# Kernel tuning notes

Hardware: AMD Instinct MI355X
Metric: run time of the kernel (lower is better)

Reference implementation:

```python
import jax, jax.numpy as jnp
import numpy as np

LOG2 = float(np.log(2.0))

def ssp(x):
    # shifted softplus: softplus(x) - log(2)
    return jax.nn.softplus(x) - LOG2

def setup_inputs() -> dict:
    key = jax.random.key(0)
    ks = jax.random.split(key, 16)
    N, E, F = 50000, 800000, 128  # atoms, interactions, feature/filter dim
    s = 0.05
    return {
        "x": jax.random.normal(ks[0], (N, F), jnp.float32),
        "dijk": jax.random.uniform(ks[1], (E, F), jnp.float32),
        "idx_j": jax.random.randint(ks[2], (E,), 0, N),
        "seg_i": jnp.sort(jax.random.randint(ks[3], (E,), 0, N)),
        "seg_j": jnp.arange(E),
        "seg_i_sum": N,
        "W1": jax.random.normal(ks[4], (F, F), jnp.float32) * s,
        "b1": jnp.zeros((F,), jnp.float32),
        "W2": jax.random.normal(ks[5], (F, F), jnp.float32) * s,
        "b2": jnp.zeros((F,), jnp.float32),
        "W_in2fac": jax.random.normal(ks[6], (F, F), jnp.float32) * s,
        "W_fac2out": jax.random.normal(ks[7], (F, F), jnp.float32) * s,
        "b_fac2out": jnp.zeros((F,), jnp.float32),
        "W_dense": jax.random.normal(ks[8], (F, F), jnp.float32) * s,
        "b_dense": jnp.zeros((F,), jnp.float32),
    }

def reference(x, dijk, idx_j, seg_i, seg_j, seg_i_sum,
              W1, b1, W2, b2, W_in2fac, W_fac2out, b_fac2out, W_dense, b_dense):
    E = dijk.shape[0]
    # --- CFnetFilter: dense -> dense -> segment-sum over seg_j ---
    h = ssp(dijk @ W1 + b1)                        # [E, F]
    w_ijk = ssp(h @ W2 + b2)                       # [E, F]
    w_ij = jax.ops.segment_sum(w_ijk, seg_j, num_segments=E)  # [E, F]
    # --- CFConv: in2fac -> gather idx_j -> filter mult -> segment-sum seg_i -> fac2out ---
    f = x @ W_in2fac                               # [N, F]
    f = f[idx_j]                                   # gather, [E, F]
    wf = w_ij * f                                  # [E, F]
    conv = jax.ops.segment_sum(wf, seg_i, num_segments=seg_i_sum)  # [N, F]
    c = ssp(conv @ W_fac2out + b_fac2out)          # [N, F]
    # --- residual dense ---
    v = c @ W_dense + b_dense                      # [N, F]
    y = x + v
    return (y, v)
```

## Files before the change

### kernel.cpp

```cpp
#include <hip/hip_runtime.h>
#include <hip/hip_bf16.h>

#define F 128

typedef __attribute__((ext_vector_type(8))) short bf16x8;
typedef __attribute__((ext_vector_type(4))) float f32x4;


__device__ __forceinline__ short f2bf(float f) {
  union { float f; unsigned u; } v; v.f = f;
  unsigned r = (v.u + 0x7FFFu + ((v.u >> 16) & 1u)) >> 16;
  return (short)r;
}

__device__ __forceinline__ float sspf(float x) {
  float t = __expf(-fabsf(x));
  return fmaxf(x, 0.0f) + __logf(1.0f + t) - 0.69314718055994530942f;
}

__device__ __forceinline__ int h_idx(int row, int k) {
  int chunk = k >> 3;
  int sw = chunk ^ (row & 15);
  return row * 128 + sw * 8 + (k & 7);
}

__device__ __forceinline__ int wf_idx(int row, int c) {
  return row * 128 + (c ^ ((row & 4) << 2));
}

__device__ __forceinline__ bf16x8 load_bfrag(const short* sW, int nt, int kb, int lane) {
  return *(const bf16x8*)(sW + (((nt * 4 + kb) * 64 + lane) << 3));
}

__device__ __forceinline__ bf16x8 load_afrag_f32(const float* __restrict__ p, bool valid) {
  bf16x8 a = {0, 0, 0, 0, 0, 0, 0, 0};
  if (valid) {
    const float4* q = (const float4*)p;
    float4 x0 = q[0], x1 = q[1];
    a[0] = f2bf(x0.x); a[1] = f2bf(x0.y); a[2] = f2bf(x0.z); a[3] = f2bf(x0.w);
    a[4] = f2bf(x1.x); a[5] = f2bf(x1.y); a[6] = f2bf(x1.z); a[7] = f2bf(x1.w);
  }
  return a;
}

__global__ void prep_weights(const float* __restrict__ W1, const float* __restrict__ W2,
                             const float* __restrict__ Wi2f, const float* __restrict__ Wf2o,
                             const float* __restrict__ Wd, unsigned short* __restrict__ out) {
  int t = blockIdx.x * 256 + threadIdx.x;
  int m = t >> 14;
  int idx = t & 16383;
  int k = idx >> 7, n = idx & 127;
  const float* W = (m == 0) ? W1 : (m == 1) ? W2 : (m == 2) ? Wi2f : (m == 3) ? Wf2o : Wd;
  float v = W[idx];
  int nt = n >> 4, kb = k >> 5;
  int lane = (((k >> 3) & 3) << 4) | (n & 15);
  int j = k & 7;
  int dst = (((nt * 4 + kb) * 64 + lane) << 3) | j;
  out[(m << 14) + dst] = (unsigned short)f2bf(v);
}

__global__ __launch_bounds__(256, 2) void f_kernel(const float* __restrict__ x,
                                                   const unsigned short* __restrict__ wfrag,
                                                   float* __restrict__ f, int N) {
  __shared__ union { short s[16384]; float4 v4[2048]; } sm;
  const int tid = threadIdx.x;
  const int lane = tid & 63, wv = tid >> 6;
  const int quad = lane >> 4, ln = lane & 15;
  const int r0 = blockIdx.x * 128;

  {
    const float4* src = (const float4*)(wfrag + 2 * 16384);
#pragma unroll
    for (int i = 0; i < 8; ++i) sm.v4[tid + 256 * i] = src[tid + 256 * i];
  }

  bf16x8 a1[2][4];
#pragma unroll
  for (int mt = 0; mt < 2; ++mt) {
    int row = r0 + wv * 32 + mt * 16 + ln;
    bool valid = row < N;
    const float* rp = x + (size_t)row * F + quad * 8;
#pragma unroll
    for (int kb = 0; kb < 4; ++kb) a1[mt][kb] = load_afrag_f32(rp + kb * 32, valid);
  }
  __syncthreads();

#pragma unroll
  for (int nt = 0; nt < 8; ++nt) {
    f32x4 acc0 = {0, 0, 0, 0}, acc1 = {0, 0, 0, 0};
#pragma unroll
    for (int kb = 0; kb < 4; ++kb) {
      bf16x8 b = load_bfrag(sm.s, nt, kb, lane);
      acc0 = __builtin_amdgcn_mfma_f32_16x16x32_bf16(a1[0][kb], b, acc0, 0, 0, 0);
      acc1 = __builtin_amdgcn_mfma_f32_16x16x32_bf16(a1[1][kb], b, acc1, 0, 0, 0);
    }
    int col = nt * 16 + ln;
#pragma unroll
    for (int mt = 0; mt < 2; ++mt) {
#pragma unroll
      for (int r = 0; r < 4; ++r) {
        int row = r0 + wv * 32 + mt * 16 + quad * 4 + r;
        if (row < N) f[(size_t)row * F + col] = (mt == 0) ? acc0[r] : acc1[r];
      }
    }
  }
}

__global__ __launch_bounds__(256, 2) void edge_kernel(
    const float* __restrict__ dijk, const int* __restrict__ idx_j, const int* __restrict__ seg_i,
    const float* __restrict__ b1, const float* __restrict__ b2,
    const unsigned short* __restrict__ wfrag, const float* __restrict__ f,
    float* __restrict__ conv, int E) {
  __shared__ union { short s[32768]; float fl[16384]; float4 v4[4096]; } sm;
  __shared__ int sIdx[128];
  __shared__ int sSeg[128];

  const int tid = threadIdx.x;
  const int lane = tid & 63, wv = tid >> 6;
  const int quad = lane >> 4, ln = lane & 15;
  const int e0 = blockIdx.x * 128;

  {
    const float4* src = (const float4*)wfrag;
#pragma unroll
    for (int i = 0; i < 16; ++i) sm.v4[tid + 256 * i] = src[tid + 256 * i];
  }
  if (tid < 128) {
    int e = e0 + tid;
    sIdx[tid] = (e < E) ? idx_j[e] : 0;
    sSeg[tid] = (e < E) ? seg_i[e] : -1;
  }

  float bias1v[8], bias2v[8];
#pragma unroll
  for (int nt = 0; nt < 8; ++nt) {
    bias1v[nt] = b1[nt * 16 + ln];
    bias2v[nt] = b2[nt * 16 + ln];
  }

  bf16x8 a1[2][4];
#pragma unroll
  for (int mt = 0; mt < 2; ++mt) {
    int row = e0 + wv * 32 + mt * 16 + ln;
    bool valid = row < E;
    const float* rp = dijk + (size_t)row * F + quad * 8;
#pragma unroll
    for (int kb = 0; kb < 4; ++kb) a1[mt][kb] = load_afrag_f32(rp + kb * 32, valid);
  }
  __syncthreads();

  short hreg[2][8][4];
  const short* sW1 = sm.s;
  const short* sW2 = sm.s + 16384;
#pragma unroll
  for (int nt = 0; nt < 8; ++nt) {
    f32x4 acc0 = {0, 0, 0, 0}, acc1 = {0, 0, 0, 0};
#pragma unroll
    for (int kb = 0; kb < 4; ++kb) {
      bf16x8 b = load_bfrag(sW1, nt, kb, lane);
      acc0 = __builtin_amdgcn_mfma_f32_16x16x32_bf16(a1[0][kb], b, acc0, 0, 0, 0);
      acc1 = __builtin_amdgcn_mfma_f32_16x16x32_bf16(a1[1][kb], b, acc1, 0, 0, 0);
    }
#pragma unroll
    for (int r = 0; r < 4; ++r) {
      hreg[0][nt][r] = f2bf(sspf(acc0[r] + bias1v[nt]));
      hreg[1][nt][r] = f2bf(sspf(acc1[r] + bias1v[nt]));
    }
  }
  __syncthreads();

  short* sH = sm.s;
#pragma unroll
  for (int mt = 0; mt < 2; ++mt)
#pragma unroll
    for (int nt = 0; nt < 8; ++nt)
#pragma unroll
      for (int r = 0; r < 4; ++r) {
        int row = wv * 32 + mt * 16 + quad * 4 + r;
        sH[h_idx(row, nt * 16 + ln)] = hreg[mt][nt][r];
      }
  __syncthreads();

  bf16x8 a2[2][4];
#pragma unroll
  for (int mt = 0; mt < 2; ++mt) {
    int row = wv * 32 + mt * 16 + ln;
#pragma unroll
    for (int kb = 0; kb < 4; ++kb)
      a2[mt][kb] = *(const bf16x8*)(sH + h_idx(row, kb * 32 + quad * 8));
  }

  float wreg[2][8][4];
#pragma unroll
  for (int nt = 0; nt < 8; ++nt) {
    f32x4 acc0 = {0, 0, 0, 0}, acc1 = {0, 0, 0, 0};
#pragma unroll
    for (int kb = 0; kb < 4; ++kb) {
      bf16x8 b = load_bfrag(sW2, nt, kb, lane);
      acc0 = __builtin_amdgcn_mfma_f32_16x16x32_bf16(a2[0][kb], b, acc0, 0, 0, 0);
      acc1 = __builtin_amdgcn_mfma_f32_16x16x32_bf16(a2[1][kb], b, acc1, 0, 0, 0);
    }
#pragma unroll
    for (int r = 0; r < 4; ++r) {
      wreg[0][nt][r] = sspf(acc0[r] + bias2v[nt]);
      wreg[1][nt][r] = sspf(acc1[r] + bias2v[nt]);
    }
  }
  __syncthreads();

  float* sWF = sm.fl;
#pragma unroll
  for (int mt = 0; mt < 2; ++mt)
#pragma unroll
    for (int r = 0; r < 4; ++r) {
      int rloc = wv * 32 + mt * 16 + quad * 4 + r;
      int jrow = sIdx[rloc];
      const float* fp = f + (size_t)jrow * F;
#pragma unroll
      for (int nt = 0; nt < 8; ++nt) {
        int c = nt * 16 + ln;
        sWF[wf_idx(rloc, c)] = wreg[mt][nt][r] * fp[c];
      }
    }
  __syncthreads();

  {
    int c = tid & 127;
    int half = tid >> 7;
    int r0 = half * 64;
    float acc = 0.0f;
    int cur = sSeg[r0];
    for (int r = r0; r < r0 + 64; ++r) {
      int s = sSeg[r];
      if (s != cur) {
        if (cur >= 0) atomicAdd(conv + (size_t)cur * F + c, acc);
        acc = 0.0f; cur = s;
      }
      acc += sWF[wf_idx(r, c)];
    }
    if (cur >= 0) atomicAdd(conv + (size_t)cur * F + c, acc);
  }
}

__global__ __launch_bounds__(256, 2) void node_kernel(
    const float* __restrict__ conv, const float* __restrict__ x,
    const float* __restrict__ bf2o, const float* __restrict__ bd,
    const unsigned short* __restrict__ wfrag, float* __restrict__ y,
    float* __restrict__ vout, int N) {
  __shared__ union { short s[32768]; float4 v4[4096]; } sm;
  const int tid = threadIdx.x;
  const int lane = tid & 63, wv = tid >> 6;
  const int quad = lane >> 4, ln = lane & 15;
  const int r0 = blockIdx.x * 128;

  {
    const float4* src = (const float4*)(wfrag + 3 * 16384);
#pragma unroll
    for (int i = 0; i < 16; ++i) sm.v4[tid + 256 * i] = src[tid + 256 * i];
  }

  float bfv[8], bdv[8];
#pragma unroll
  for (int nt = 0; nt < 8; ++nt) {
    bfv[nt] = bf2o[nt * 16 + ln];
    bdv[nt] = bd[nt * 16 + ln];
  }

  bf16x8 a1[2][4];
#pragma unroll
  for (int mt = 0; mt < 2; ++mt) {
    int row = r0 + wv * 32 + mt * 16 + ln;
    bool valid = row < N;
    const float* rp = conv + (size_t)row * F + quad * 8;
#pragma unroll
    for (int kb = 0; kb < 4; ++kb) a1[mt][kb] = load_afrag_f32(rp + kb * 32, valid);
  }
  __syncthreads();

  short creg[2][8][4];
  const short* sWa = sm.s;
  const short* sWd = sm.s + 16384;
#pragma unroll
  for (int nt = 0; nt < 8; ++nt) {
    f32x4 acc0 = {0, 0, 0, 0}, acc1 = {0, 0, 0, 0};
#pragma unroll
    for (int kb = 0; kb < 4; ++kb) {
      bf16x8 b = load_bfrag(sWa, nt, kb, lane);
      acc0 = __builtin_amdgcn_mfma_f32_16x16x32_bf16(a1[0][kb], b, acc0, 0, 0, 0);
      acc1 = __builtin_amdgcn_mfma_f32_16x16x32_bf16(a1[1][kb], b, acc1, 0, 0, 0);
    }
#pragma unroll
    for (int r = 0; r < 4; ++r) {
      creg[0][nt][r] = f2bf(sspf(acc0[r] + bfv[nt]));
      creg[1][nt][r] = f2bf(sspf(acc1[r] + bfv[nt]));
    }
  }
  __syncthreads();

  short* sC = sm.s;
#pragma unroll
  for (int mt = 0; mt < 2; ++mt)
#pragma unroll
    for (int nt = 0; nt < 8; ++nt)
#pragma unroll
      for (int r = 0; r < 4; ++r) {
        int row = wv * 32 + mt * 16 + quad * 4 + r;
        sC[h_idx(row, nt * 16 + ln)] = creg[mt][nt][r];
      }
  __syncthreads();

  bf16x8 a2[2][4];
#pragma unroll
  for (int mt = 0; mt < 2; ++mt) {
    int row = wv * 32 + mt * 16 + ln;
#pragma unroll
    for (int kb = 0; kb < 4; ++kb)
      a2[mt][kb] = *(const bf16x8*)(sC + h_idx(row, kb * 32 + quad * 8));
  }

#pragma unroll
  for (int nt = 0; nt < 8; ++nt) {
    f32x4 acc0 = {0, 0, 0, 0}, acc1 = {0, 0, 0, 0};
#pragma unroll
    for (int kb = 0; kb < 4; ++kb) {
      bf16x8 b = load_bfrag(sWd, nt, kb, lane);
      acc0 = __builtin_amdgcn_mfma_f32_16x16x32_bf16(a2[0][kb], b, acc0, 0, 0, 0);
      acc1 = __builtin_amdgcn_mfma_f32_16x16x32_bf16(a2[1][kb], b, acc1, 0, 0, 0);
    }
    int col = nt * 16 + ln;
#pragma unroll
    for (int mt = 0; mt < 2; ++mt) {
#pragma unroll
      for (int r = 0; r < 4; ++r) {
        int row = r0 + wv * 32 + mt * 16 + quad * 4 + r;
        if (row < N) {
          float v = ((mt == 0) ? acc0[r] : acc1[r]) + bdv[nt];
          size_t o = (size_t)row * F + col;
          y[o] = x[o] + v;
          vout[o] = v;
        }
      }
    }
  }
}

extern "C" void kernel_launch(void* const* d_in, const int* in_sizes, int n_in,
                              void* d_out, int out_size, void* d_ws, size_t ws_size,
                              hipStream_t stream) {
  const float* x    = (const float*)d_in[0];
  const float* dijk = (const float*)d_in[1];
  const int*   idxj = (const int*)d_in[2];
  const int*   segi = (const int*)d_in[3];
  const float* W1   = (const float*)d_in[6];
  const float* b1   = (const float*)d_in[7];
  const float* W2   = (const float*)d_in[8];
  const float* b2   = (const float*)d_in[9];
  const float* Wi2f = (const float*)d_in[10];
  const float* Wf2o = (const float*)d_in[11];
  const float* bf2o = (const float*)d_in[12];
  const float* Wd   = (const float*)d_in[13];
  const float* bd   = (const float*)d_in[14];

  int N = in_sizes[0] / F;
  int E = in_sizes[1] / F;

  unsigned short* wfrag = (unsigned short*)d_ws;
  float* fbuf = (float*)((char*)d_ws + 5 * 16384 * sizeof(unsigned short));
  float* conv = fbuf + (size_t)N * F;

  float* y = (float*)d_out;
  float* vout = y + (size_t)N * F;

  hipMemsetAsync(conv, 0, (size_t)N * F * sizeof(float), stream);
  prep_weights<<<320, 256, 0, stream>>>(W1, W2, Wi2f, Wf2o, Wd, wfrag);

  int nb = (N + 127) / 128;
  int eb = (E + 127) / 128;
  f_kernel<<<nb, 256, 0, stream>>>(x, wfrag, fbuf, N);
  edge_kernel<<<eb, 256, 0, stream>>>(dijk, idxj, segi, b1, b2, wfrag, fbuf, conv, E);
  node_kernel<<<nb, 256, 0, stream>>>(conv, x, bf2o, bd, wfrag, y, vout, N);
}
```

Baseline: 844.9 us.

## Read weight fragments from global memory and halve LDS to raise occupancy

```diff
diff --git a/kernel.cpp b/kernel.cpp
--- a/kernel.cpp
+++ b/kernel.cpp
@@ -1,5 +1,4 @@
 #include <hip/hip_runtime.h>
-#include <hip/hip_bf16.h>
 
 #define F 128
 
@@ -13,6 +12,12 @@
   return (short)r;
 }
 
+__device__ __forceinline__ unsigned cvt_pk_bf16(float a, float b) {
+  unsigned d;
+  asm("v_cvt_pk_bf16_f32 %0, %1, %2" : "=v"(d) : "v"(a), "v"(b));
+  return d;
+}
+
 __device__ __forceinline__ float sspf(float x) {
   float t = __expf(-fabsf(x));
   return fmaxf(x, 0.0f) + __logf(1.0f + t) - 0.69314718055994530942f;
@@ -24,23 +29,28 @@
   return row * 128 + sw * 8 + (k & 7);
 }
 
-__device__ __forceinline__ int wf_idx(int row, int c) {
+__device__ __forceinline__ int wfb_idx(int row, int c) {
   return row * 128 + (c ^ ((row & 4) << 2));
 }
 
-__device__ __forceinline__ bf16x8 load_bfrag(const short* sW, int nt, int kb, int lane) {
-  return *(const bf16x8*)(sW + (((nt * 4 + kb) * 64 + lane) << 3));
+__device__ __forceinline__ bf16x8 load_bfrag_g(const unsigned short* __restrict__ W,
+                                               int nt, int kb, int lane) {
+  return *(const bf16x8*)(W + (((nt * 4 + kb) * 64 + lane) << 3));
 }
 
 __device__ __forceinline__ bf16x8 load_afrag_f32(const float* __restrict__ p, bool valid) {
-  bf16x8 a = {0, 0, 0, 0, 0, 0, 0, 0};
+  union { bf16x8 v; unsigned u[4]; } r;
   if (valid) {
     const float4* q = (const float4*)p;
     float4 x0 = q[0], x1 = q[1];
-    a[0] = f2bf(x0.x); a[1] = f2bf(x0.y); a[2] = f2bf(x0.z); a[3] = f2bf(x0.w);
-    a[4] = f2bf(x1.x); a[5] = f2bf(x1.y); a[6] = f2bf(x1.z); a[7] = f2bf(x1.w);
-  }
-  return a;
+    r.u[0] = cvt_pk_bf16(x0.x, x0.y);
+    r.u[1] = cvt_pk_bf16(x0.z, x0.w);
+    r.u[2] = cvt_pk_bf16(x1.x, x1.y);
+    r.u[3] = cvt_pk_bf16(x1.z, x1.w);
+  } else {
+    r.u[0] = r.u[1] = r.u[2] = r.u[3] = 0u;
+  }
+  return r.v;
 }
 
 __global__ void prep_weights(const float* __restrict__ W1, const float* __restrict__ W2,
@@ -59,20 +69,14 @@
   out[(m << 14) + dst] = (unsigned short)f2bf(v);
 }
 
-__global__ __launch_bounds__(256, 2) void f_kernel(const float* __restrict__ x,
+__global__ __launch_bounds__(256, 4) void f_kernel(const float* __restrict__ x,
                                                    const unsigned short* __restrict__ wfrag,
                                                    float* __restrict__ f, int N) {
-  __shared__ union { short s[16384]; float4 v4[2048]; } sm;
   const int tid = threadIdx.x;
   const int lane = tid & 63, wv = tid >> 6;
   const int quad = lane >> 4, ln = lane & 15;
   const int r0 = blockIdx.x * 128;
-
-  {
-    const float4* src = (const float4*)(wfrag + 2 * 16384);
-#pragma unroll
-    for (int i = 0; i < 8; ++i) sm.v4[tid + 256 * i] = src[tid + 256 * i];
-  }
+  const unsigned short* Wf = wfrag + 2 * 16384;
 
   bf16x8 a1[2][4];
 #pragma unroll
@@ -83,14 +87,13 @@
 #pragma unroll
     for (int kb = 0; kb < 4; ++kb) a1[mt][kb] = load_afrag_f32(rp + kb * 32, valid);
   }
-  __syncthreads();
-
-#pragma unroll
-  for (int nt = 0; nt < 8; ++nt) {
-    f32x4 acc0 = {0, 0, 0, 0}, acc1 = {0, 0, 0, 0};
-#pragma unroll
-    for (int kb = 0; kb < 4; ++kb) {
-      bf16x8 b = load_bfrag(sm.s, nt, kb, lane);
+
+#pragma unroll
+  for (int nt = 0; nt < 8; ++nt) {
+    f32x4 acc0 = {0, 0, 0, 0}, acc1 = {0, 0, 0, 0};
+#pragma unroll
+    for (int kb = 0; kb < 4; ++kb) {
+      bf16x8 b = load_bfrag_g(Wf, nt, kb, lane);
       acc0 = __builtin_amdgcn_mfma_f32_16x16x32_bf16(a1[0][kb], b, acc0, 0, 0, 0);
       acc1 = __builtin_amdgcn_mfma_f32_16x16x32_bf16(a1[1][kb], b, acc1, 0, 0, 0);
     }
@@ -106,12 +109,12 @@
   }
 }
 
-__global__ __launch_bounds__(256, 2) void edge_kernel(
+__global__ __launch_bounds__(256, 4) void edge_kernel(
     const float* __restrict__ dijk, const int* __restrict__ idx_j, const int* __restrict__ seg_i,
     const float* __restrict__ b1, const float* __restrict__ b2,
     const unsigned short* __restrict__ wfrag, const float* __restrict__ f,
     float* __restrict__ conv, int E) {
-  __shared__ union { short s[32768]; float fl[16384]; float4 v4[4096]; } sm;
+  __shared__ union { short s[16384]; float fl[8192]; } sm;
   __shared__ int sIdx[128];
   __shared__ int sSeg[128];
 
@@ -119,12 +122,9 @@
   const int lane = tid & 63, wv = tid >> 6;
   const int quad = lane >> 4, ln = lane & 15;
   const int e0 = blockIdx.x * 128;
-
-  {
-    const float4* src = (const float4*)wfrag;
-#pragma unroll
-    for (int i = 0; i < 16; ++i) sm.v4[tid + 256 * i] = src[tid + 256 * i];
-  }
+  const unsigned short* W1f = wfrag;
+  const unsigned short* W2f = wfrag + 16384;
+
   if (tid < 128) {
     int e = e0 + tid;
     sIdx[tid] = (e < E) ? idx_j[e] : 0;
@@ -147,38 +147,26 @@
 #pragma unroll
     for (int kb = 0; kb < 4; ++kb) a1[mt][kb] = load_afrag_f32(rp + kb * 32, valid);
   }
-  __syncthreads();
-
-  short hreg[2][8][4];
-  const short* sW1 = sm.s;
-  const short* sW2 = sm.s + 16384;
-#pragma unroll
-  for (int nt = 0; nt < 8; ++nt) {
-    f32x4 acc0 = {0, 0, 0, 0}, acc1 = {0, 0, 0, 0};
-#pragma unroll
-    for (int kb = 0; kb < 4; ++kb) {
-      bf16x8 b = load_bfrag(sW1, nt, kb, lane);
+
+  short* sH = sm.s;
+#pragma unroll
+  for (int nt = 0; nt < 8; ++nt) {
+    f32x4 acc0 = {0, 0, 0, 0}, acc1 = {0, 0, 0, 0};
+#pragma unroll
+    for (int kb = 0; kb < 4; ++kb) {
+      bf16x8 b = load_bfrag_g(W1f, nt, kb, lane);
       acc0 = __builtin_amdgcn_mfma_f32_16x16x32_bf16(a1[0][kb], b, acc0, 0, 0, 0);
       acc1 = __builtin_amdgcn_mfma_f32_16x16x32_bf16(a1[1][kb], b, acc1, 0, 0, 0);
     }
+    int c = nt * 16 + ln;
 #pragma unroll
     for (int r = 0; r < 4; ++r) {
-      hreg[0][nt][r] = f2bf(sspf(acc0[r] + bias1v[nt]));
-      hreg[1][nt][r] = f2bf(sspf(acc1[r] + bias1v[nt]));
-    }
-  }
-  __syncthreads();
-
-  short* sH = sm.s;
-#pragma unroll
-  for (int mt = 0; mt < 2; ++mt)
-#pragma unroll
-    for (int nt = 0; nt < 8; ++nt)
-#pragma unroll
-      for (int r = 0; r < 4; ++r) {
-        int row = wv * 32 + mt * 16 + quad * 4 + r;
-        sH[h_idx(row, nt * 16 + ln)] = hreg[mt][nt][r];
-      }
+      sH[h_idx(wv * 32 + quad * 4 + r, c)] =
+          (short)cvt_pk_bf16(sspf(acc0[r] + bias1v[nt]), 0.0f);
+      sH[h_idx(wv * 32 + 16 + quad * 4 + r, c)] =
+          (short)cvt_pk_bf16(sspf(acc1[r] + bias1v[nt]), 0.0f);
+    }
+  }
   __syncthreads();
 
   bf16x8 a2[2][4];
@@ -196,7 +184,7 @@
     f32x4 acc0 = {0, 0, 0, 0}, acc1 = {0, 0, 0, 0};
 #pragma unroll
     for (int kb = 0; kb < 4; ++kb) {
-      bf16x8 b = load_bfrag(sW2, nt, kb, lane);
+      bf16x8 b = load_bfrag_g(W2f, nt, kb, lane);
       acc0 = __builtin_amdgcn_mfma_f32_16x16x32_bf16(a2[0][kb], b, acc0, 0, 0, 0);
       acc1 = __builtin_amdgcn_mfma_f32_16x16x32_bf16(a2[1][kb], b, acc1, 0, 0, 0);
     }
@@ -210,54 +198,55 @@
 
   float* sWF = sm.fl;
 #pragma unroll
-  for (int mt = 0; mt < 2; ++mt)
+  for (int half = 0; half < 2; ++half) {
 #pragma unroll
     for (int r = 0; r < 4; ++r) {
-      int rloc = wv * 32 + mt * 16 + quad * 4 + r;
-      int jrow = sIdx[rloc];
+      int lr = quad * 4 + r;
+      int brow = wv * 16 + lr;
+      int erow = wv * 32 + half * 16 + lr;
+      int jrow = sIdx[erow];
       const float* fp = f + (size_t)jrow * F;
 #pragma unroll
       for (int nt = 0; nt < 8; ++nt) {
         int c = nt * 16 + ln;
-        sWF[wf_idx(rloc, c)] = wreg[mt][nt][r] * fp[c];
+        sWF[wfb_idx(brow, c)] = wreg[half][nt][r] * fp[c];
       }
     }
-  __syncthreads();
-
-  {
-    int c = tid & 127;
-    int half = tid >> 7;
-    int r0 = half * 64;
-    float acc = 0.0f;
-    int cur = sSeg[r0];
-    for (int r = r0; r < r0 + 64; ++r) {
-      int s = sSeg[r];
-      if (s != cur) {
-        if (cur >= 0) atomicAdd(conv + (size_t)cur * F + c, acc);
-        acc = 0.0f; cur = s;
+    __syncthreads();
+
+    {
+      int c = tid & 127;
+      int sub = tid >> 7;
+      int b0 = sub * 32;
+      float acc = 0.0f;
+      int cur = sSeg[((b0 >> 4) << 5) + half * 16 + (b0 & 15)];
+      for (int b = b0; b < b0 + 32; ++b) {
+        int act = ((b >> 4) << 5) + half * 16 + (b & 15);
+        int s = sSeg[act];
+        if (s != cur) {
+          if (cur >= 0) atomicAdd(conv + (size_t)cur * F + c, acc);
+          acc = 0.0f; cur = s;
+        }
+        acc += sWF[wfb_idx(b, c)];
       }
-      acc += sWF[wf_idx(r, c)];
-    }
-    if (cur >= 0) atomicAdd(conv + (size_t)cur * F + c, acc);
-  }
-}
-
-__global__ __launch_bounds__(256, 2) void node_kernel(
+      if (cur >= 0) atomicAdd(conv + (size_t)cur * F + c, acc);
+    }
+    if (half == 0) __syncthreads();
+  }
+}
+
+__global__ __launch_bounds__(256, 4) void node_kernel(
     const float* __restrict__ conv, const float* __restrict__ x,
     const float* __restrict__ bf2o, const float* __restrict__ bd,
     const unsigned short* __restrict__ wfrag, float* __restrict__ y,
     float* __restrict__ vout, int N) {
-  __shared__ union { short s[32768]; float4 v4[4096]; } sm;
+  __shared__ short sC[16384];
   const int tid = threadIdx.x;
   const int lane = tid & 63, wv = tid >> 6;
   const int quad = lane >> 4, ln = lane & 15;
   const int r0 = blockIdx.x * 128;
-
-  {
-    const float4* src = (const float4*)(wfrag + 3 * 16384);
-#pragma unroll
-    for (int i = 0; i < 16; ++i) sm.v4[tid + 256 * i] = src[tid + 256 * i];
-  }
+  const unsigned short* Wa = wfrag + 3 * 16384;
+  const unsigned short* Wd = wfrag + 4 * 16384;
 
   float bfv[8], bdv[8];
 #pragma unroll
@@ -275,38 +264,25 @@
 #pragma unroll
     for (int kb = 0; kb < 4; ++kb) a1[mt][kb] = load_afrag_f32(rp + kb * 32, valid);
   }
-  __syncthreads();
-
-  short creg[2][8][4];
-  const short* sWa = sm.s;
-  const short* sWd = sm.s + 16384;
-#pragma unroll
-  for (int nt = 0; nt < 8; ++nt) {
-    f32x4 acc0 = {0, 0, 0, 0}, acc1 = {0, 0, 0, 0};
-#pragma unroll
-    for (int kb = 0; kb < 4; ++kb) {
-      bf16x8 b = load_bfrag(sWa, nt, kb, lane);
+
+#pragma unroll
+  for (int nt = 0; nt < 8; ++nt) {
+    f32x4 acc0 = {0, 0, 0, 0}, acc1 = {0, 0, 0, 0};
+#pragma unroll
+    for (int kb = 0; kb < 4; ++kb) {
+      bf16x8 b = load_bfrag_g(Wa, nt, kb, lane);
       acc0 = __builtin_amdgcn_mfma_f32_16x16x32_bf16(a1[0][kb], b, acc0, 0, 0, 0);
       acc1 = __builtin_amdgcn_mfma_f32_16x16x32_bf16(a1[1][kb], b, acc1, 0, 0, 0);
     }
+    int c = nt * 16 + ln;
 #pragma unroll
     for (int r = 0; r < 4; ++r) {
-      creg[0][nt][r] = f2bf(sspf(acc0[r] + bfv[nt]));
-      creg[1][nt][r] = f2bf(sspf(acc1[r] + bfv[nt]));
-    }
-  }
-  __syncthreads();
-
-  short* sC = sm.s;
-#pragma unroll
-  for (int mt = 0; mt < 2; ++mt)
-#pragma unroll
-    for (int nt = 0; nt < 8; ++nt)
-#pragma unroll
-      for (int r = 0; r < 4; ++r) {
-        int row = wv * 32 + mt * 16 + quad * 4 + r;
-        sC[h_idx(row, nt * 16 + ln)] = creg[mt][nt][r];
-      }
+      sC[h_idx(wv * 32 + quad * 4 + r, c)] =
+          (short)cvt_pk_bf16(sspf(acc0[r] + bfv[nt]), 0.0f);
+      sC[h_idx(wv * 32 + 16 + quad * 4 + r, c)] =
+          (short)cvt_pk_bf16(sspf(acc1[r] + bfv[nt]), 0.0f);
+    }
+  }
   __syncthreads();
 
   bf16x8 a2[2][4];
@@ -323,7 +299,7 @@
     f32x4 acc0 = {0, 0, 0, 0}, acc1 = {0, 0, 0, 0};
 #pragma unroll
     for (int kb = 0; kb < 4; ++kb) {
-      bf16x8 b = load_bfrag(sWd, nt, kb, lane);
+      bf16x8 b = load_bfrag_g(Wd, nt, kb, lane);
       acc0 = __builtin_amdgcn_mfma_f32_16x16x32_bf16(a2[0][kb], b, acc0, 0, 0, 0);
       acc1 = __builtin_amdgcn_mfma_f32_16x16x32_bf16(a2[1][kb], b, acc1, 0, 0, 0);
     }
```

Result: slower. 907.9 us (+7.5%).
